# Optimization experiments

Hardware: AMD Instinct MI355X
Metric: run time of the kernel (lower is better)

The kernel has to match this reference:

```python
import jax, jax.numpy as jnp
import numpy as np

EPS = 1e-5


def _conv(x, k, pad):
    # x: (B,C,H,W), k: (Co,Ci,kh,kw)
    return jax.lax.conv_general_dilated(
        x, k, window_strides=(1, 1), padding=pad,
        dimension_numbers=("NCHW", "OIHW", "NCHW"))


def _prop_rows(x, k, b, g, bt, m, v, a, reverse):
    # direction 'D' (reverse=False) or 'U' (reverse=True).
    # conv on a 1xW stripe with 3x3 pad1 only uses the middle kernel row.
    kmid = k[:, :, 1:2, :]  # (C,C,1,3)
    # conv(current + res) = (K*current + b) + K*res ; precompute per-row part.
    pre = _conv(x, kmid, [(0, 0), (1, 1)]) + b[None, :, None, None]  # (B,C,H,W)
    inv = g / jnp.sqrt(v + EPS)
    mn, bn_b = m[None, :, None], bt[None, :, None]
    inv3 = inv[None, :, None]

    def step(res, pre_i):  # res, pre_i: (B,C,W)
        h = pre_i + _conv(res[:, :, None, :], kmid, [(0, 0), (1, 1)])[:, :, 0, :]
        y = (h - mn) * inv3 + bn_b
        y = jnp.where(y >= 0, y, a * y)  # PReLU (single shared param)
        return y, y

    B, _, H, W = x.shape
    res0 = jnp.zeros((B, k.shape[0], W), x.dtype)
    xs = jnp.moveaxis(pre, 2, 0)  # (H,B,C,W)
    _, ys = jax.lax.scan(step, res0, xs, reverse=reverse)
    return jnp.moveaxis(ys, 0, 2)  # (B,C,H,W)


def _prop_cols(x, k, b, g, bt, m, v, a, reverse):
    # direction 'R' (reverse=False) or 'L' (reverse=True); only middle kernel col used.
    kmid = k[:, :, :, 1:2]  # (C,C,3,1)
    pre = _conv(x, kmid, [(1, 1), (0, 0)]) + b[None, :, None, None]  # (B,C,H,W)
    inv = g / jnp.sqrt(v + EPS)
    mn, bn_b = m[None, :, None], bt[None, :, None]
    inv3 = inv[None, :, None]

    def step(res, pre_i):  # res, pre_i: (B,C,H)
        h = pre_i + _conv(res[:, :, :, None], kmid, [(1, 1), (0, 0)])[:, :, :, 0]
        y = (h - mn) * inv3 + bn_b
        y = jnp.where(y >= 0, y, a * y)
        return y, y

    B, _, H, W = x.shape
    res0 = jnp.zeros((B, k.shape[0], H), x.dtype)
    xs = jnp.moveaxis(pre, 3, 0)  # (W,B,C,H)
    _, ys = jax.lax.scan(step, res0, xs, reverse=reverse)
    return jnp.moveaxis(ys, 0, 3)  # (B,C,H,W)


def setup_inputs() -> dict:
    key = jax.random.key(0)
    ks = jax.random.split(key, 16)
    B, C, H, W = 8, 128, 160, 160
    x = jax.random.normal(ks[0], (B, C, H, W), jnp.float32)
    # std ~ 1/sqrt(fan_in=C*3) keeps the recurrence stable
    kernels = jax.random.normal(ks[1], (4, C, C, 3, 3), jnp.float32) * 0.04
    biases = jax.random.normal(ks[2], (4, C), jnp.float32) * 0.05
    bn_gamma = 1.0 + 0.1 * jax.random.normal(ks[3], (4, C), jnp.float32)
    bn_beta = 0.1 * jax.random.normal(ks[4], (4, C), jnp.float32)
    bn_mean = 0.1 * jax.random.normal(ks[5], (4, C), jnp.float32)
    bn_var = 1.0 + 0.1 * jax.random.uniform(ks[6], (4, C), jnp.float32)
    prelu_a = jnp.full((4,), 0.25, jnp.float32)
    fus_w = jax.random.normal(ks[7], (C, 4 * C), jnp.float32) * 0.04
    fus_b = jax.random.normal(ks[8], (C,), jnp.float32) * 0.05
    fbn_gamma = 1.0 + 0.1 * jax.random.normal(ks[9], (C,), jnp.float32)
    fbn_beta = 0.1 * jax.random.normal(ks[10], (C,), jnp.float32)
    fbn_mean = 0.1 * jax.random.normal(ks[11], (C,), jnp.float32)
    fbn_var = 1.0 + 0.1 * jax.random.uniform(ks[12], (C,), jnp.float32)
    return dict(x=x, kernels=kernels, biases=biases, bn_gamma=bn_gamma,
                bn_beta=bn_beta, bn_mean=bn_mean, bn_var=bn_var,
                prelu_a=prelu_a, fus_w=fus_w, fus_b=fus_b,
                fbn_gamma=fbn_gamma, fbn_beta=fbn_beta, fbn_mean=fbn_mean,
                fbn_var=fbn_var)


def reference(x, kernels, biases, bn_gamma, bn_beta, bn_mean, bn_var, prelu_a,
              fus_w, fus_b, fbn_gamma, fbn_beta, fbn_mean, fbn_var):
    def p(i):
        return (kernels[i], biases[i], bn_gamma[i], bn_beta[i], bn_mean[i],
                bn_var[i], prelu_a[i])

    feat_D = _prop_rows(x, *p(0), reverse=False)
    feat_U = _prop_rows(x, *p(1), reverse=True)
    feat_R = _prop_cols(x, *p(2), reverse=False)
    feat_L = _prop_cols(x, *p(3), reverse=True)
    feat = jnp.concatenate([feat_D, feat_U, feat_R, feat_L], axis=1)  # (B,4C,H,W)
    out = jnp.einsum("oc,bchw->bohw", fus_w, feat) + fus_b[None, :, None, None]
    inv = fbn_gamma / jnp.sqrt(fbn_var + EPS)
    out = (out - fbn_mean[None, :, None, None]) * inv[None, :, None, None] \
        + fbn_beta[None, :, None, None]
    return jax.nn.relu(out)
```

## Files before the change

### kernel.cpp

```cpp
#include <hip/hip_runtime.h>
#include <stdint.h>


typedef __attribute__((ext_vector_type(8))) __bf16 bf16x8;
typedef __attribute__((ext_vector_type(4))) float f32x4;

#define DEV static __device__ __forceinline__

DEV unsigned short f2bf(float f) {
  union { float f; unsigned int u; } v; v.f = f;
  unsigned int u = v.u;
  u += 0x7fffu + ((u >> 16) & 1u);
  return (unsigned short)(u >> 16);
}
DEV float bf2f(unsigned short s) {
  union { float f; unsigned int u; } v; v.u = ((unsigned int)s) << 16;
  return v.f;
}
DEV f32x4 mfma16(bf16x8 a, bf16x8 b, f32x4 c) {
  return __builtin_amdgcn_mfma_f32_16x16x32_bf16(a, b, c, 0, 0, 0);
}
DEV void barrier_lds() {
  asm volatile("s_waitcnt lgkmcnt(0)\n\ts_barrier" ::: "memory");
}

constexpr int Hc = 160, Wc = 160, Cc = 128;
constexpr int CHUNK = 16, NCH = 10;
constexpr int ROWS = 18;
constexpr int SPAD = 136;

constexpr long WS_XT    = 0;
constexpr long WS_WPREP = 104857600;
constexpr long WS_EPI   = 105250816;
constexpr long WS_FWT   = 105254912;
constexpr long WS_FEPI  = 105385984;
constexpr long WS_FEAT  = 105387008;
constexpr long WS_EX    = 315102208;
constexpr long WS_TOTAL = 315757568;

__global__ void prep_kernel(const float* __restrict__ kern, const float* __restrict__ bias,
                            const float* __restrict__ bg, const float* __restrict__ bb,
                            const float* __restrict__ bm, const float* __restrict__ bv,
                            const float* __restrict__ fw, const float* __restrict__ fb2,
                            const float* __restrict__ fg, const float* __restrict__ fbt,
                            const float* __restrict__ fm, const float* __restrict__ fv,
                            unsigned short* __restrict__ wprep, float2* __restrict__ epi,
                            unsigned short* __restrict__ fwT, float2* __restrict__ fepi)
{
  int idx = blockIdx.x * 256 + threadIdx.x;
  if (idx < 196608) {
    int c = idx & 127;
    int t = (idx >> 7) % 3;
    int o = (idx / 384) & 127;
    int d = idx / 49152;
    int kh = (d < 2) ? 1 : t;
    int kw = (d < 2) ? t : 1;
    wprep[idx] = f2bf(kern[(((d * 128 + o) * 128 + c) * 3 + kh) * 3 + kw]);
  }
  int i2 = idx - 196608;
  if (i2 >= 0 && i2 < 65536) fwT[i2] = f2bf(fw[i2]);
  int i3 = idx - 262144;
  if (i3 >= 0 && i3 < 512) {
    float sc = bg[i3] / sqrtf(bv[i3] + 1e-5f);
    epi[i3] = make_float2(sc, (bias[i3] - bm[i3]) * sc + bb[i3]);
  }
  int i4 = idx - 262656;
  if (i4 >= 0 && i4 < 128) {
    float sc = fg[i4] / sqrtf(fv[i4] + 1e-5f);
    fepi[i4] = make_float2(sc, (fb2[i4] - fm[i4]) * sc + fbt[i4]);
  }
}

__global__ void transpose_kernel(const float* __restrict__ x, float* __restrict__ xT)
{
  __shared__ float tile[32][33];
  int b = blockIdx.z, h = blockIdx.y;
  int c0 = (blockIdx.x / 5) * 32, w0 = (blockIdx.x % 5) * 32;
  int tx = threadIdx.x & 31, ty = threadIdx.x >> 5;
#pragma unroll
  for (int r = 0; r < 4; r++) {
    int c = c0 + ty + 8 * r;
    tile[ty + 8 * r][tx] = x[(((long)b * 128 + c) * 160 + h) * 160 + w0 + tx];
  }
  __syncthreads();
#pragma unroll
  for (int r = 0; r < 4; r++) {
    int w = w0 + ty + 8 * r;
    xT[(((long)b * 160 + h) * 160 + w) * 128 + c0 + tx] = tile[tx][ty + 8 * r];
  }
}

#define SCAN_STEP(T, PAR, XC, XHC, XN, XHN)                                     \
  do {                                                                          \
    const int t_ = (T);                                                         \
    const int i_ = rev ? (159 - t_) : t_;                                       \
    const bool last_ = (t_ == 159);                                             \
    const unsigned short* cur_ = sbuf[s][PAR];                                  \
    unsigned short* nxt_ = sbuf[s][(PAR) ^ 1];                                  \
        \
    if (t_ < 158) {                                                             \
      const float* xr2_ = xb + (long)(rev ? (i_ - 2) : (i_ + 2)) * si;          \
      _Pragma("unroll") for (int j = 0; j < 2; j++)                             \
        _Pragma("unroll") for (int r = 0; r < 4; r++)                           \
          XN[j][r] = xr2_[xoff[j][r]];                                          \
      if (ug_ok) XHN = xr2_[xhoff];                                             \
    }                                                                           \
          \
    f32x4 acc0_ = {0.f, 0.f, 0.f, 0.f}, acc1_ = {0.f, 0.f, 0.f, 0.f};           \
    _Pragma("unroll") for (int kt = 0; kt < 12; kt++) {                         \
      const int tt_ = kt >> 2;                                                  \
      const int cc_ = ((kt & 3) << 5) + (kq << 3);                              \
      const bf16x8 A0_ = *(const bf16x8*)&cur_[(ncol + tt_) * SPAD + cc_];      \
      acc0_ = mfma16(A0_, Bfrag[0][kt], acc0_);                                 \
      acc1_ = mfma16(A0_, Bfrag[1][kt], acc1_);                                 \
    }                                                                           \
                                                 \
    float yf_[2][4];                                                            \
    unsigned short yb_[2][4];                                                   \
    _Pragma("unroll") for (int r = 0; r < 4; r++) {                             \
      float v0_ = acc0_[r] * ep[0].x + ep[0].y;                                 \
      v0_ = (v0_ >= 0.f) ? v0_ : (aslope * v0_);                                \
      yf_[0][r] = v0_; yb_[0][r] = f2bf(v0_);                                   \
      float v1_ = acc1_[r] * ep[1].x + ep[1].y;                                 \
      v1_ = (v1_ >= 0.f) ? v1_ : (aslope * v1_);                                \
      yf_[1][r] = v1_; yb_[1][r] = f2bf(v1_);                                   \
    }                                                                           \
                    \
    {                                                                           \
      const unsigned int tagv_ = ((unsigned int)(t_ + 1)) << 16;                \
      if (kq == 0) {                                                            \
        __hip_atomic_store(&ex_self[(PAR) * 128 + colj[0]],                     \
                           tagv_ | (unsigned int)yb_[0][0],                     \
                           __ATOMIC_RELAXED, __HIP_MEMORY_SCOPE_AGENT);         \
        __hip_atomic_store(&ex_self[(PAR) * 128 + colj[1]],                     \
                           tagv_ | (unsigned int)yb_[1][0],                     \
                           __ATOMIC_RELAXED, __HIP_MEMORY_SCOPE_AGENT);         \
      }                                                                         \
      if (kq == 3) {                                                            \
        __hip_atomic_store(&ex_self[256 + (PAR) * 128 + colj[0]],               \
                           tagv_ | (unsigned int)yb_[0][3],                     \
                           __ATOMIC_RELAXED, __HIP_MEMORY_SCOPE_AGENT);         \
        __hip_atomic_store(&ex_self[256 + (PAR) * 128 + colj[1]],               \
                           tagv_ | (unsigned int)yb_[1][3],                     \
                           __ATOMIC_RELAXED, __HIP_MEMORY_SCOPE_AGENT);         \
      }                                                                         \
    }                                                                           \
                  \
    unsigned int hv_ = 0;                                                       \
    if (!last_ && interior)                                                     \
      hv_ = __hip_atomic_load(ex_nbr + (PAR) * 128 + oh,                        \
                              __ATOMIC_RELAXED, __HIP_MEMORY_SCOPE_AGENT);      \
               \
    if (!last_) {                                                               \
      _Pragma("unroll") for (int j = 0; j < 2; j++)                             \
        _Pragma("unroll") for (int r = 0; r < 4; r++)                           \
          nxt_[(1 + kq * 4 + r) * SPAD + colj[j]] =                             \
              f2bf(XC[j][r] + yf_[j][r]);                                       \
    }                                                                           \
                  \
    {                                                                           \
      unsigned short* frow_ = fbp + (long)i_ * fi;                              \
      _Pragma("unroll") for (int j = 0; j < 2; j++)                             \
        _Pragma("unroll") for (int r = 0; r < 4; r++)                           \
          frow_[foff[j][r]] = yb_[j][r];                                        \
    }                                                                           \
        \
    if (!last_) {                                                               \
      float yv_ = 0.f;                                                          \
      if (interior) {                                                           \
        const unsigned int* slot_ = ex_nbr + (PAR) * 128 + oh;                  \
        unsigned int v_ = hv_;                                                  \
        while ((v_ >> 16) != (unsigned int)(t_ + 1)) {                          \
          __builtin_amdgcn_s_sleep(1);                                          \
          v_ = __hip_atomic_load(slot_, __ATOMIC_RELAXED,                       \
                                 __HIP_MEMORY_SCOPE_AGENT);                     \
        }                                                                       \
        yv_ = bf2f((unsigned short)(v_ & 0xffffu));                             \
      }                                                                         \
      unsigned short sv_ = 0;                                                   \
      if (ug_ok) sv_ = f2bf(XHC + yv_);                                         \
      nxt_[srow * SPAD + oh] = sv_;                                             \
    }                                                                           \
    barrier_lds();  \
  } while (0)

__global__ __launch_bounds__(512, 2) void scan_kernel(
    const float* __restrict__ xT, const unsigned short* __restrict__ wprep,
    const float2* __restrict__ epi, const float* __restrict__ prelu_a,
    unsigned short* __restrict__ featbuf, unsigned int* __restrict__ ex)
{
  __shared__ __align__(16) unsigned short sbuf[2][2][ROWS * SPAD];

  const int bid = blockIdx.x;
  const int q = bid >> 4;
  const int g = bid & 15;
  const int p = g >> 3, b = g & 7;
  const int tid = threadIdx.x;
  const int wv = tid >> 6;
  const int s = wv >> 2;
  const int wl = wv & 3;
  const int lane = tid & 63;
  const int ncol = lane & 15;
  const int kq = lane >> 4;
  const int d = p * 2 + s;
  const bool rev = (s != 0);
  const int u0 = q * CHUNK;

  const bool row_mode = (p == 0);
  const long si = row_mode ? (long)Wc * Cc : (long)Cc;
  const int  su = row_mode ? Cc : Wc * Cc;
  const long fi = row_mode ? (long)Wc * 512 : (long)512;
  const int  fu = row_mode ? 512 : Wc * 512;
  const float* xb = xT + (long)b * Hc * Wc * Cc;
  unsigned short* fbp = featbuf + (long)b * Hc * Wc * 512 + d * 128;

  bf16x8 Bfrag[2][12];
  float2 ep[2];
  int colj[2];
#pragma unroll
  for (int j = 0; j < 2; j++) {
    const int o = (wl * 2 + j) * 16 + ncol;
    colj[j] = o;
    const unsigned short* wp = wprep + ((long)(d * 128 + o)) * 384;
#pragma unroll
    for (int kt = 0; kt < 12; kt++)
      Bfrag[j][kt] = *(const bf16x8*)(wp + kt * 32 + kq * 8);
    ep[j] = epi[d * 128 + o];
  }
  const float aslope = prelu_a[d];

  int xoff[2][4], foff[2][4];
#pragma unroll
  for (int j = 0; j < 2; j++)
#pragma unroll
    for (int r = 0; r < 4; r++) {
      const int row = kq * 4 + r;
      xoff[j][r] = (u0 + row) * su + colj[j];
      foff[j][r] = (u0 + row) * fu + colj[j];
    }

  const int sid = d * 80 + b * 10 + q;
  unsigned int* ex_self = ex + (long)sid * 512;

  const int hside = (tid >> 7) & 1;
  const int oh = tid & 127;
  const bool interior = hside ? (q < NCH - 1) : (q > 0);
  const int ug = hside ? (u0 + CHUNK) : (u0 - 1);
  const bool ug_ok = (ug >= 0 && ug < 160);
  const int srow = hside ? (ROWS - 1) : 0;
  const int xhoff = ug_ok ? (ug * su + oh) : 0;
  const unsigned int* ex_nbr = hside ? (ex + (long)(sid + 1) * 512)
                                     : (ex + (long)(sid - 1) * 512 + 256);

  const int i0 = rev ? (Hc - 1) : 0;
  const int tids = tid & 255;
  for (int e = tids; e < ROWS * 64; e += 256) {
    const int u = e >> 6, cp = e & 63;
    const int uu = u0 + u - 1;
    unsigned int sv = 0;
    if (uu >= 0 && uu < 160) {
      const float2 xv2 = *(const float2*)(xb + (long)i0 * si + (long)uu * su + cp * 2);
      sv = (unsigned int)f2bf(xv2.x) | ((unsigned int)f2bf(xv2.y) << 16);
    }
    *(unsigned int*)&sbuf[s][0][u * SPAD + cp * 2] = sv;
  }

  float xcA[2][4], xcB[2][4];
  float xhA = 0.f, xhB = 0.f;
  {
    const float* xrow = xb + (long)(rev ? (Hc - 2) : 1) * si;
#pragma unroll
    for (int j = 0; j < 2; j++)
#pragma unroll
      for (int r = 0; r < 4; r++)
        xcA[j][r] = xrow[xoff[j][r]];
    if (ug_ok) xhA = xrow[xhoff];
  }
#pragma unroll
  for (int j = 0; j < 2; j++)
#pragma unroll
    for (int r = 0; r < 4; r++) xcB[j][r] = 0.f;

  barrier_lds();

#pragma unroll 1
  for (int tb = 0; tb < 160; tb += 2) {
    SCAN_STEP(tb,     0, xcA, xhA, xcB, xhB);
    SCAN_STEP(tb + 1, 1, xcB, xhB, xcA, xhA);
  }
}
#undef SCAN_STEP

__global__ __launch_bounds__(256, 1) void fusion_kernel(
    const unsigned short* __restrict__ featbuf, const unsigned short* __restrict__ fwT,
    const float2* __restrict__ fepi, float* __restrict__ out)
{
  __shared__ unsigned short At[32 * 520];
  const int bx = blockIdx.x;
  const int b = bx / 800, mb = bx - b * 800;
  const long m0 = (long)mb * 32;
  const int tid = threadIdx.x, lane = tid & 63, wv = tid >> 6;
  const int ncol = lane & 15, kq = lane >> 4;

  const unsigned short* fp = featbuf + ((long)b * 25600 + m0) * 512;
#pragma unroll
  for (int rr = 0; rr < 8; rr++) {
    const int e = tid + rr * 256;
    const int m = e >> 6, kp = e & 63;
    *(bf16x8*)&At[m * 520 + kp * 8] = *(const bf16x8*)(fp + (long)m * 512 + kp * 8);
  }
  bf16x8 Bf[2][16];
  float2 fe[2];
#pragma unroll
  for (int j = 0; j < 2; j++) {
    const int o = (wv * 2 + j) * 16 + ncol;
    const unsigned short* wp = fwT + (long)o * 512;
#pragma unroll
    for (int kt = 0; kt < 16; kt++)
      Bf[j][kt] = *(const bf16x8*)(wp + kt * 32 + kq * 8);
    fe[j] = fepi[o];
  }
  __syncthreads();

  f32x4 acc[2][2];
#pragma unroll
  for (int mt = 0; mt < 2; mt++)
#pragma unroll
    for (int j = 0; j < 2; j++)
      acc[mt][j] = (f32x4){0.f, 0.f, 0.f, 0.f};
#pragma unroll
  for (int kt = 0; kt < 16; kt++) {
    const bf16x8 A0 = *(const bf16x8*)&At[ncol * 520 + kt * 32 + kq * 8];
    const bf16x8 A1 = *(const bf16x8*)&At[(16 + ncol) * 520 + kt * 32 + kq * 8];
    acc[0][0] = mfma16(A0, Bf[0][kt], acc[0][0]);
    acc[0][1] = mfma16(A0, Bf[1][kt], acc[0][1]);
    acc[1][0] = mfma16(A1, Bf[0][kt], acc[1][0]);
    acc[1][1] = mfma16(A1, Bf[1][kt], acc[1][1]);
  }
#pragma unroll
  for (int mt = 0; mt < 2; mt++)
#pragma unroll
    for (int j = 0; j < 2; j++) {
      const int o = (wv * 2 + j) * 16 + ncol;
      const long hw = m0 + mt * 16 + kq * 4;
      f32x4 v;
#pragma unroll
      for (int r = 0; r < 4; r++) {
        const float z = acc[mt][j][r] * fe[j].x + fe[j].y;
        v[r] = (z > 0.f) ? z : 0.f;
      }
      *(f32x4*)(out + ((long)(b * 128 + o)) * 25600 + hw) = v;
    }
}

extern "C" void kernel_launch(void* const* d_in, const int* in_sizes, int n_in,
                              void* d_out, int out_size, void* d_ws, size_t ws_size,
                              hipStream_t stream)
{
  if (ws_size < (size_t)WS_TOTAL) return;

  const float* x        = (const float*)d_in[0];
  const float* kernels  = (const float*)d_in[1];
  const float* biases   = (const float*)d_in[2];
  const float* bn_gamma = (const float*)d_in[3];
  const float* bn_beta  = (const float*)d_in[4];
  const float* bn_mean  = (const float*)d_in[5];
  const float* bn_var   = (const float*)d_in[6];
  const float* prelu_a  = (const float*)d_in[7];
  const float* fus_w    = (const float*)d_in[8];
  const float* fus_b    = (const float*)d_in[9];
  const float* fbn_g    = (const float*)d_in[10];
  const float* fbn_b    = (const float*)d_in[11];
  const float* fbn_m    = (const float*)d_in[12];
  const float* fbn_v    = (const float*)d_in[13];

  char* ws = (char*)d_ws;
  float*          xT      = (float*)(ws + WS_XT);
  unsigned short* wprep   = (unsigned short*)(ws + WS_WPREP);
  float2*         epi     = (float2*)(ws + WS_EPI);
  unsigned short* fwT     = (unsigned short*)(ws + WS_FWT);
  float2*         fepi    = (float2*)(ws + WS_FEPI);
  unsigned short* featbuf = (unsigned short*)(ws + WS_FEAT);
  unsigned int*   ex      = (unsigned int*)(ws + WS_EX);
  float*          out     = (float*)d_out;

  prep_kernel<<<1027, 256, 0, stream>>>(kernels, biases, bn_gamma, bn_beta, bn_mean, bn_var,
                                        fus_w, fus_b, fbn_g, fbn_b, fbn_m, fbn_v,
                                        wprep, epi, fwT, fepi);
  transpose_kernel<<<dim3(20, 160, 8), 256, 0, stream>>>(x, xT);
  scan_kernel<<<160, 512, 0, stream>>>(xT, wprep, epi, prelu_a, featbuf, ex);
  fusion_kernel<<<6400, 256, 0, stream>>>(featbuf, fwT, fepi, out);
}
```

Baseline: 598.7 us.

## Use overlapping halo chunks to exchange boundaries every eight scan steps

```diff
diff --git a/kernel.cpp b/kernel.cpp
--- a/kernel.cpp
+++ b/kernel.cpp
@@ -25,8 +25,8 @@
 }
 
 constexpr int Hc = 160, Wc = 160, Cc = 128;
-constexpr int CHUNK = 16, NCH = 10;
-constexpr int ROWS = 18;
+constexpr int CHUNK = 32, NCH = 5;
+constexpr int SR = 50;
 constexpr int SPAD = 136;
 
 constexpr long WS_XT    = 0;
@@ -35,8 +35,8 @@
 constexpr long WS_FWT   = 105254912;
 constexpr long WS_FEPI  = 105385984;
 constexpr long WS_FEAT  = 105387008;
-constexpr long WS_EX    = 315102208;
-constexpr long WS_TOTAL = 315757568;
+constexpr long WS_TOTAL = 315102208;
+constexpr int EX_WORDS = 160 * 2 * 8 * 128;
 
 __global__ void prep_kernel(const float* __restrict__ kern, const float* __restrict__ bias,
                             const float* __restrict__ bg, const float* __restrict__ bb,
@@ -45,9 +45,11 @@
                             const float* __restrict__ fg, const float* __restrict__ fbt,
                             const float* __restrict__ fm, const float* __restrict__ fv,
                             unsigned short* __restrict__ wprep, float2* __restrict__ epi,
-                            unsigned short* __restrict__ fwT, float2* __restrict__ fepi)
+                            unsigned short* __restrict__ fwT, float2* __restrict__ fepi,
+                            unsigned int* __restrict__ exz)
 {
   int idx = blockIdx.x * 256 + threadIdx.x;
+  if (idx < EX_WORDS) exz[idx] = 0;
   if (idx < 196608) {
     int c = idx & 127;
     int t = (idx >> 7) % 3;
@@ -90,123 +92,126 @@
   }
 }
 
-#define SCAN_STEP(T, PAR, XC, XHC, XN, XHN)                                     \
+#define SCAN_STEP(T, PAR, PUB)                                                  \
   do {                                                                          \
     const int t_ = (T);                                                         \
     const int i_ = rev ? (159 - t_) : t_;                                       \
     const bool last_ = (t_ == 159);                                             \
-    const unsigned short* cur_ = sbuf[s][PAR];                                  \
-    unsigned short* nxt_ = sbuf[s][(PAR) ^ 1];                                  \
-        \
-    if (t_ < 158) {                                                             \
-      const float* xr2_ = xb + (long)(rev ? (i_ - 2) : (i_ + 2)) * si;          \
-      _Pragma("unroll") for (int j = 0; j < 2; j++)                             \
+    const unsigned short* cur_ = sbuf[PAR];                                     \
+    unsigned short* nxt_ = sbuf[(PAR) ^ 1];                                     \
+               \
+    if (!last_) {                                                               \
+      const float* xr_ = xb + (long)(rev ? (i_ - 1) : (i_ + 1)) * si;           \
+      _Pragma("unroll") for (int m = 0; m < 3; m++)                             \
         _Pragma("unroll") for (int r = 0; r < 4; r++)                           \
-          XN[j][r] = xr2_[xoff[j][r]];                                          \
-      if (ug_ok) XHN = xr2_[xhoff];                                             \
-    }                                                                           \
-          \
-    f32x4 acc0_ = {0.f, 0.f, 0.f, 0.f}, acc1_ = {0.f, 0.f, 0.f, 0.f};           \
+          xn[m][r] = xr_[xoff[m][r]];                                           \
+    }                                                                           \
+           \
+    f32x4 acc[3];                                                               \
+    acc[0] = (f32x4){0.f, 0.f, 0.f, 0.f};                                       \
+    acc[1] = (f32x4){0.f, 0.f, 0.f, 0.f};                                       \
+    acc[2] = (f32x4){0.f, 0.f, 0.f, 0.f};                                       \
     _Pragma("unroll") for (int kt = 0; kt < 12; kt++) {                         \
       const int tt_ = kt >> 2;                                                  \
       const int cc_ = ((kt & 3) << 5) + (kq << 3);                              \
-      const bf16x8 A0_ = *(const bf16x8*)&cur_[(ncol + tt_) * SPAD + cc_];      \
-      acc0_ = mfma16(A0_, Bfrag[0][kt], acc0_);                                 \
-      acc1_ = mfma16(A0_, Bfrag[1][kt], acc1_);                                 \
+      _Pragma("unroll") for (int m = 0; m < 3; m++) {                           \
+        const bf16x8 A_ = *(const bf16x8*)&cur_[(m * 16 + ncol + tt_) * SPAD + cc_]; \
+        acc[m] = mfma16(A_, Bfrag[kt], acc[m]);                                 \
+      }                                                                         \
     }                                                                           \
                                                  \
-    float yf_[2][4];                                                            \
-    unsigned short yb_[2][4];                                                   \
-    _Pragma("unroll") for (int r = 0; r < 4; r++) {                             \
-      float v0_ = acc0_[r] * ep[0].x + ep[0].y;                                 \
-      v0_ = (v0_ >= 0.f) ? v0_ : (aslope * v0_);                                \
-      yf_[0][r] = v0_; yb_[0][r] = f2bf(v0_);                                   \
-      float v1_ = acc1_[r] * ep[1].x + ep[1].y;                                 \
-      v1_ = (v1_ >= 0.f) ? v1_ : (aslope * v1_);                                \
-      yf_[1][r] = v1_; yb_[1][r] = f2bf(v1_);                                   \
-    }                                                                           \
-                    \
-    {                                                                           \
-      const unsigned int tagv_ = ((unsigned int)(t_ + 1)) << 16;                \
-      if (kq == 0) {                                                            \
-        __hip_atomic_store(&ex_self[(PAR) * 128 + colj[0]],                     \
-                           tagv_ | (unsigned int)yb_[0][0],                     \
+    _Pragma("unroll") for (int m = 0; m < 3; m++)                               \
+      _Pragma("unroll") for (int r = 0; r < 4; r++) {                           \
+        float v_ = acc[m][r] * ep.x + ep.y;                                     \
+        v_ = (v_ >= 0.f) ? v_ : (aslope * v_);                                  \
+        yf[m][r] = v_; yb[m][r] = f2bf(v_);                                     \
+      }                                                                         \
+                      \
+    if (PUB) {                                                                  \
+      const unsigned int tagv_ = ((unsigned int)((t_ + 1) >> 3)) << 16;         \
+      _Pragma("unroll") for (int r = 0; r < 4; r++) {                           \
+        const unsigned int pv_ = (kq >= 2) ? (unsigned int)yb[0][r]             \
+                                           : (unsigned int)yb[2][r];            \
+        __hip_atomic_store(pubp + r * 128, tagv_ | pv_,                         \
                            __ATOMIC_RELAXED, __HIP_MEMORY_SCOPE_AGENT);         \
-        __hip_atomic_store(&ex_self[(PAR) * 128 + colj[1]],                     \
-                           tagv_ | (unsigned int)yb_[1][0],                     \
-                           __ATOMIC_RELAXED, __HIP_MEMORY_SCOPE_AGENT);         \
-      }                                                                         \
-      if (kq == 3) {                                                            \
-        __hip_atomic_store(&ex_self[256 + (PAR) * 128 + colj[0]],               \
-                           tagv_ | (unsigned int)yb_[0][3],                     \
-                           __ATOMIC_RELAXED, __HIP_MEMORY_SCOPE_AGENT);         \
-        __hip_atomic_store(&ex_self[256 + (PAR) * 128 + colj[1]],               \
-                           tagv_ | (unsigned int)yb_[1][3],                     \
-                           __ATOMIC_RELAXED, __HIP_MEMORY_SCOPE_AGENT);         \
-      }                                                                         \
-    }                                                                           \
-                  \
-    unsigned int hv_ = 0;                                                       \
-    if (!last_ && interior)                                                     \
-      hv_ = __hip_atomic_load(ex_nbr + (PAR) * 128 + oh,                        \
-                              __ATOMIC_RELAXED, __HIP_MEMORY_SCOPE_AGENT);      \
+      }                                                                         \
+    }                                                                           \
                \
     if (!last_) {                                                               \
-      _Pragma("unroll") for (int j = 0; j < 2; j++)                             \
-        _Pragma("unroll") for (int r = 0; r < 4; r++)                           \
-          nxt_[(1 + kq * 4 + r) * SPAD + colj[j]] =                             \
-              f2bf(XC[j][r] + yf_[j][r]);                                       \
-    }                                                                           \
-                  \
+      _Pragma("unroll") for (int m = 0; m < 3; m++)                             \
+        _Pragma("unroll") for (int r = 0; r < 4; r++) {                         \
+          unsigned short sv_ = 0;                                               \
+          if (xok[m][r]) sv_ = f2bf(xn[m][r] + yf[m][r]);                       \
+          nxt_[(m * 16 + kq * 4 + r + 1) * SPAD + o] = sv_;                     \
+        }                                                                       \
+    }                                                                           \
+                             \
     {                                                                           \
       unsigned short* frow_ = fbp + (long)i_ * fi;                              \
-      _Pragma("unroll") for (int j = 0; j < 2; j++)                             \
-        _Pragma("unroll") for (int r = 0; r < 4; r++)                           \
-          frow_[foff[j][r]] = yb_[j][r];                                        \
-    }                                                                           \
-        \
-    if (!last_) {                                                               \
-      float yv_ = 0.f;                                                          \
-      if (interior) {                                                           \
-        const unsigned int* slot_ = ex_nbr + (PAR) * 128 + oh;                  \
-        unsigned int v_ = hv_;                                                  \
-        while ((v_ >> 16) != (unsigned int)(t_ + 1)) {                          \
+      _Pragma("unroll") for (int r = 0; r < 4; r++) {                           \
+        frow_[foff0[r]] = yb[1][r];                                             \
+        frow_[foff1[r]] = (kq >= 2) ? yb[0][r] : yb[2][r];                      \
+      }                                                                         \
+    }                                                                           \
+    barrier_lds();                                                              \
+  } while (0)
+
+#define EXCH_FILL(T, PARN)                                                      \
+  do {                                                                          \
+    const int tn_ = (T) + 1;                                                    \
+    const unsigned int e_ = (unsigned int)(tn_ >> 3);                           \
+    const int in_ = rev ? (159 - tn_) : tn_;                                    \
+    unsigned short* nxt_ = sbuf[PARN];                                          \
+    const float* xr_ = xb + (long)in_ * si;                                     \
+    _Pragma("unroll") for (int k = 0; k < 4; k++) {                             \
+      const int c_ = tid + (k << 9);                                            \
+      const int side_ = c_ >> 10;                                               \
+      const int rr_ = (c_ >> 7) & 7;                                            \
+      const int ch_ = c_ & 127;                                                 \
+      const int u_ = side_ ? (u0 + 32 + rr_) : (u0 - 8 + rr_);                  \
+      const int lsp_ = side_ ? (41 + rr_) : (rr_ + 1);                          \
+      unsigned short sv_ = 0;                                                   \
+      if (u_ >= 0 && u_ < 160) {                                                \
+        const unsigned int* slot_ = exbase +                                    \
+            (long)(side_ ? (sid + 1) : (sid - 1)) * 2048 +                      \
+            (((side_ ^ 1) << 3) + rr_) * 128 + ch_;                             \
+        const float xv_ = xr_[u_ * su + ch_];                                   \
+        unsigned int v_ = __hip_atomic_load(slot_, __ATOMIC_RELAXED,            \
+                                            __HIP_MEMORY_SCOPE_AGENT);          \
+        while ((v_ >> 16) != e_) {                                              \
           __builtin_amdgcn_s_sleep(1);                                          \
           v_ = __hip_atomic_load(slot_, __ATOMIC_RELAXED,                       \
                                  __HIP_MEMORY_SCOPE_AGENT);                     \
         }                                                                       \
-        yv_ = bf2f((unsigned short)(v_ & 0xffffu));                             \
-      }                                                                         \
-      unsigned short sv_ = 0;                                                   \
-      if (ug_ok) sv_ = f2bf(XHC + yv_);                                         \
-      nxt_[srow * SPAD + oh] = sv_;                                             \
-    }                                                                           \
-    barrier_lds();  \
+        sv_ = f2bf(xv_ + bf2f((unsigned short)(v_ & 0xffffu)));                 \
+      }                                                                         \
+      nxt_[lsp_ * SPAD + ch_] = sv_;                                            \
+    }                                                                           \
+    barrier_lds();                                                              \
   } while (0)
 
-__global__ __launch_bounds__(512, 2) void scan_kernel(
+__global__ __launch_bounds__(512, 1) void scan_kernel(
     const float* __restrict__ xT, const unsigned short* __restrict__ wprep,
     const float2* __restrict__ epi, const float* __restrict__ prelu_a,
-    unsigned short* __restrict__ featbuf, unsigned int* __restrict__ ex)
-{
-  __shared__ __align__(16) unsigned short sbuf[2][2][ROWS * SPAD];
+    unsigned short* __restrict__ featbuf, unsigned int* exbase)
+{
+  __shared__ __align__(16) unsigned short sbuf[2][SR * SPAD];
 
   const int bid = blockIdx.x;
-  const int q = bid >> 4;
-  const int g = bid & 15;
-  const int p = g >> 3, b = g & 7;
+  const int q = bid >> 5;
+  const int g = bid & 31;
+  const int d = g >> 3;
+  const int b = g & 7;
   const int tid = threadIdx.x;
   const int wv = tid >> 6;
-  const int s = wv >> 2;
-  const int wl = wv & 3;
   const int lane = tid & 63;
   const int ncol = lane & 15;
   const int kq = lane >> 4;
-  const int d = p * 2 + s;
-  const bool rev = (s != 0);
+  const int o = wv * 16 + ncol;
+  const bool rev = (d & 1);
   const int u0 = q * CHUNK;
 
-  const bool row_mode = (p == 0);
+  const bool row_mode = (d < 2);
   const long si = row_mode ? (long)Wc * Cc : (long)Cc;
   const int  su = row_mode ? Cc : Wc * Cc;
   const long fi = row_mode ? (long)Wc * 512 : (long)512;
@@ -214,82 +219,65 @@
   const float* xb = xT + (long)b * Hc * Wc * Cc;
   unsigned short* fbp = featbuf + (long)b * Hc * Wc * 512 + d * 128;
 
-  bf16x8 Bfrag[2][12];
-  float2 ep[2];
-  int colj[2];
-#pragma unroll
-  for (int j = 0; j < 2; j++) {
-    const int o = (wl * 2 + j) * 16 + ncol;
-    colj[j] = o;
+  bf16x8 Bfrag[12];
+  {
     const unsigned short* wp = wprep + ((long)(d * 128 + o)) * 384;
 #pragma unroll
     for (int kt = 0; kt < 12; kt++)
-      Bfrag[j][kt] = *(const bf16x8*)(wp + kt * 32 + kq * 8);
-    ep[j] = epi[d * 128 + o];
-  }
+      Bfrag[kt] = *(const bf16x8*)(wp + kt * 32 + kq * 8);
+  }
+  const float2 ep = epi[d * 128 + o];
   const float aslope = prelu_a[d];
 
-  int xoff[2][4], foff[2][4];
-#pragma unroll
-  for (int j = 0; j < 2; j++)
+  int xoff[3][4]; bool xok[3][4];
+#pragma unroll
+  for (int m = 0; m < 3; m++)
 #pragma unroll
     for (int r = 0; r < 4; r++) {
-      const int row = kq * 4 + r;
-      xoff[j][r] = (u0 + row) * su + colj[j];
-      foff[j][r] = (u0 + row) * fu + colj[j];
+      const int u = u0 - 8 + m * 16 + kq * 4 + r;
+      const bool ok = (u >= 0 && u < 160);
+      xok[m][r] = ok;
+      xoff[m][r] = (ok ? u : 0) * su + o;
     }
-
-  const int sid = d * 80 + b * 10 + q;
-  unsigned int* ex_self = ex + (long)sid * 512;
-
-  const int hside = (tid >> 7) & 1;
-  const int oh = tid & 127;
-  const bool interior = hside ? (q < NCH - 1) : (q > 0);
-  const int ug = hside ? (u0 + CHUNK) : (u0 - 1);
-  const bool ug_ok = (ug >= 0 && ug < 160);
-  const int srow = hside ? (ROWS - 1) : 0;
-  const int xhoff = ug_ok ? (ug * su + oh) : 0;
-  const unsigned int* ex_nbr = hside ? (ex + (long)(sid + 1) * 512)
-                                     : (ex + (long)(sid - 1) * 512 + 256);
+  int foff0[4], foff1[4];
+#pragma unroll
+  for (int r = 0; r < 4; r++) {
+    foff0[r] = (u0 + 8 + kq * 4 + r) * fu + o;
+    const int u1 = (kq >= 2) ? (u0 + (kq - 2) * 4 + r)
+                             : (u0 + 24 + kq * 4 + r);
+    foff1[r] = u1 * fu + o;
+  }
+
+  const int sid = d * 40 + b * 5 + q;
+  unsigned int* exw = exbase + (long)sid * 2048;
+  unsigned int* pubp = exw + (((kq >= 2) ? (0 * 8 + (kq - 2) * 4)
+                                         : (1 * 8 + kq * 4)) * 128 + o);
 
   const int i0 = rev ? (Hc - 1) : 0;
-  const int tids = tid & 255;
-  for (int e = tids; e < ROWS * 64; e += 256) {
-    const int u = e >> 6, cp = e & 63;
-    const int uu = u0 + u - 1;
+  for (int e = tid; e < SR * 64; e += 512) {
+    const int lsp = e >> 6, cp = e & 63;
+    const int u = u0 - 9 + lsp;
     unsigned int sv = 0;
-    if (uu >= 0 && uu < 160) {
-      const float2 xv2 = *(const float2*)(xb + (long)i0 * si + (long)uu * su + cp * 2);
+    if (u >= 0 && u < 160) {
+      const float2 xv2 = *(const float2*)(xb + (long)i0 * si + (long)u * su + cp * 2);
       sv = (unsigned int)f2bf(xv2.x) | ((unsigned int)f2bf(xv2.y) << 16);
     }
-    *(unsigned int*)&sbuf[s][0][u * SPAD + cp * 2] = sv;
-  }
-
-  float xcA[2][4], xcB[2][4];
-  float xhA = 0.f, xhB = 0.f;
-  {
-    const float* xrow = xb + (long)(rev ? (Hc - 2) : 1) * si;
-#pragma unroll
-    for (int j = 0; j < 2; j++)
-#pragma unroll
-      for (int r = 0; r < 4; r++)
-        xcA[j][r] = xrow[xoff[j][r]];
-    if (ug_ok) xhA = xrow[xhoff];
-  }
-#pragma unroll
-  for (int j = 0; j < 2; j++)
-#pragma unroll
-    for (int r = 0; r < 4; r++) xcB[j][r] = 0.f;
-
+    *(unsigned int*)&sbuf[0][lsp * SPAD + cp * 2] = sv;
+  }
   barrier_lds();
 
+  float yf[3][4]; unsigned short yb[3][4]; float xn[3][4];
+
 #pragma unroll 1
-  for (int tb = 0; tb < 160; tb += 2) {
-    SCAN_STEP(tb,     0, xcA, xhA, xcB, xhB);
-    SCAN_STEP(tb + 1, 1, xcB, xhB, xcA, xhA);
+  for (int t = 0; t < 160; t += 2) {
+    SCAN_STEP(t, 0, false);
+    const bool ex = ((t & 7) == 6) && (t != 158);
+    SCAN_STEP(t + 1, 1, ex);
+    if (ex) EXCH_FILL(t + 1, 0);
   }
 }
 #undef SCAN_STEP
+#undef EXCH_FILL
 
 __global__ __launch_bounds__(256, 1) void fusion_kernel(
     const unsigned short* __restrict__ featbuf, const unsigned short* __restrict__ fwT,
@@ -381,12 +369,12 @@
   unsigned short* fwT     = (unsigned short*)(ws + WS_FWT);
   float2*         fepi    = (float2*)(ws + WS_FEPI);
   unsigned short* featbuf = (unsigned short*)(ws + WS_FEAT);
-  unsigned int*   ex      = (unsigned int*)(ws + WS_EX);
+  unsigned int*   ex      = (unsigned int*)d_out;
   float*          out     = (float*)d_out;
 
-  prep_kernel<<<1027, 256, 0, stream>>>(kernels, biases, bn_gamma, bn_beta, bn_mean, bn_var,
+  prep_kernel<<<1280, 256, 0, stream>>>(kernels, biases, bn_gamma, bn_beta, bn_mean, bn_var,
                                         fus_w, fus_b, fbn_g, fbn_b, fbn_m, fbn_v,
-                                        wprep, epi, fwT, fepi);
+                                        wprep, epi, fwT, fepi, ex);
   transpose_kernel<<<dim3(20, 160, 8), 256, 0, stream>>>(x, xT);
   scan_kernel<<<160, 512, 0, stream>>>(xT, wprep, epi, prelu_a, featbuf, ex);
   fusion_kernel<<<6400, 256, 0, stream>>>(featbuf, fwT, fepi, out);
```

Result: slower. 651.8 us (+8.9%).
